# Optimization experiments

Hardware: AMD Instinct MI355X
Metric: run time of the kernel (lower is better)

Reference implementation:

```python
import jax, jax.numpy as jnp
import numpy as np

B_SZ, CH, H, W = 32, 256, 28, 28
D_INNER, D_STATE, D_CONV, DT_RANK, DEPTH = 512, 16, 4, 16, 2


def setup_inputs() -> dict:
    key = jax.random.key(0)
    ks = jax.random.split(key, 10)
    s = 0.02
    A = jnp.broadcast_to(jnp.arange(1, D_STATE + 1, dtype=jnp.float32), (DEPTH, D_INNER, D_STATE))
    return {
        "bbox_feats": jax.random.normal(ks[0], (B_SZ, CH, H, W), jnp.float32),
        "norm_w": jnp.ones((DEPTH, CH), jnp.float32),
        "norm_b": jnp.zeros((DEPTH, CH), jnp.float32),
        "in_proj_w": jax.random.normal(ks[1], (DEPTH, 2 * D_INNER, CH), jnp.float32) * s,
        "conv_w": jax.random.normal(ks[2], (DEPTH, D_INNER, D_CONV), jnp.float32) * 0.1,
        "conv_b": jnp.zeros((DEPTH, D_INNER), jnp.float32),
        "x_proj_w": jax.random.normal(ks[3], (DEPTH, DT_RANK + 2 * D_STATE, D_INNER), jnp.float32) * s,
        "dt_proj_w": jax.random.normal(ks[4], (DEPTH, D_INNER, DT_RANK), jnp.float32) * 0.1,
        "dt_proj_b": jax.random.normal(ks[5], (DEPTH, D_INNER), jnp.float32) * 0.1,
        "A_log": jnp.log(A),
        "D_param": jnp.ones((DEPTH, D_INNER), jnp.float32),
        "out_proj_w": jax.random.normal(ks[6], (DEPTH, CH, D_INNER), jnp.float32) * s,
    }


def _layernorm(x, w, b, eps=1e-5):
    mu = jnp.mean(x, axis=-1, keepdims=True)
    var = jnp.mean(jnp.square(x - mu), axis=-1, keepdims=True)
    return (x - mu) * jax.lax.rsqrt(var + eps) * w + b


def _mamba(x, in_w, cw, cb, xp_w, dtp_w, dtp_b, A_log, Dp, out_w):
    # x: [B, L, d_model]
    B, L, _ = x.shape
    xz = jnp.einsum('bld,ed->ble', x, in_w)          # [B, L, 2*d_inner]
    xi, z = jnp.split(xz, 2, axis=-1)                # each [B, L, d_inner]
    # depthwise causal conv1d (kernel D_CONV, left pad D_CONV-1)
    xpad = jnp.pad(xi, ((0, 0), (D_CONV - 1, 0), (0, 0)))
    xc = cb
    for k in range(D_CONV):
        xc = xc + xpad[:, k:k + L, :] * cw[:, k]
    xc = jax.nn.silu(xc)                             # [B, L, d_inner]
    x_dbl = jnp.einsum('bld,ed->ble', xc, xp_w)      # [B, L, dt_rank+2*d_state]
    dt_r = x_dbl[..., :DT_RANK]
    Bm = x_dbl[..., DT_RANK:DT_RANK + D_STATE]
    Cm = x_dbl[..., DT_RANK + D_STATE:]
    dt = jax.nn.softplus(jnp.einsum('blr,dr->bld', dt_r, dtp_w) + dtp_b)  # [B, L, d_inner]
    A = -jnp.exp(A_log)                              # [d_inner, d_state]

    def step(h, inp):
        dt_t, B_t, C_t, x_t = inp                    # [B,d_inner],[B,d_state],[B,d_state],[B,d_inner]
        dA = jnp.exp(dt_t[:, :, None] * A)           # [B, d_inner, d_state]
        h = h * dA + dt_t[:, :, None] * B_t[:, None, :] * x_t[:, :, None]
        y = jnp.einsum('bds,bs->bd', h, C_t)
        return h, y

    h0 = jnp.zeros((B, D_INNER, D_STATE), x.dtype)
    inputs = (jnp.swapaxes(dt, 0, 1), jnp.swapaxes(Bm, 0, 1),
              jnp.swapaxes(Cm, 0, 1), jnp.swapaxes(xc, 0, 1))
    _, ys = jax.lax.scan(step, h0, inputs)
    y = jnp.swapaxes(ys, 0, 1) + xc * Dp             # [B, L, d_inner]
    y = y * jax.nn.silu(z)
    return jnp.einsum('bld,ed->ble', y, out_w)       # [B, L, d_model]


def reference(bbox_feats, norm_w, norm_b, in_proj_w, conv_w, conv_b,
              x_proj_w, dt_proj_w, dt_proj_b, A_log, D_param, out_proj_w):
    B, C, h, w = bbox_feats.shape
    x = bbox_feats
    for i in range(DEPTH):
        xf = jnp.swapaxes(x.reshape(B, C, h * w), -1, -2)   # [B, L, C]
        xn = _layernorm(xf, norm_w[i], norm_b[i])
        ym = _mamba(xn, in_proj_w[i], conv_w[i], conv_b[i], x_proj_w[i],
                    dt_proj_w[i], dt_proj_b[i], A_log[i], D_param[i], out_proj_w[i])
        x = jnp.swapaxes(ym, -1, -2).reshape(B, C, h, w)
    return x
```

## Files before the change

kernel.cpp:

```cpp
#include <hip/hip_runtime.h>
#include <cstdint>
#include <cstddef>

#define BSZ  32
#define CHN  256
#define LSEQ 784
#define DI   512
#define NCH  16

typedef unsigned short u16;
typedef short s16x8 __attribute__((ext_vector_type(8)));
typedef float f32x4 __attribute__((ext_vector_type(4)));

__device__ __forceinline__ float b2f(u16 u) {
  union { unsigned int i; float f; } v; v.i = ((unsigned int)u) << 16; return v.f;
}
__device__ __forceinline__ u16 f2b(float f) {
  union { float f; unsigned int i; } v; v.f = f;
  unsigned int x = v.i;
  return (u16)((x + 0x7FFFu + ((x >> 16) & 1u)) >> 16);
}

#define SA_HALF(dv, xv, Q0, Q1, Q2, Q3) do {                                  \
  float dx_ = (dv) * (xv);                                                    \
  float w1_ = __expf(-(dv));                                                  \
  float e2_ = w1_*w1_, e4_ = e2_*e2_, e8_ = e4_*e4_;                          \
  float p3_ = e2_*w1_, p5_ = e4_*w1_, p6_ = e4_*e2_, p7_ = p6_*w1_;           \
  float p9_ = e8_*w1_, p10_ = e8_*e2_, p11_ = p10_*w1_, p12_ = e8_*e4_;       \
  float p13_ = p12_*w1_, p14_ = p12_*e2_, p15_ = p14_*w1_, p16_ = e8_*e8_;    \
  h[0]  = h[0]*w1_  + dx_*Q0.x;  h[1]  = h[1]*e2_  + dx_*Q0.y;                \
  h[2]  = h[2]*p3_  + dx_*Q0.z;  h[3]  = h[3]*e4_  + dx_*Q0.w;                \
  h[4]  = h[4]*p5_  + dx_*Q1.x;  h[5]  = h[5]*p6_  + dx_*Q1.y;                \
  h[6]  = h[6]*p7_  + dx_*Q1.z;  h[7]  = h[7]*e8_  + dx_*Q1.w;                \
  h[8]  = h[8]*p9_  + dx_*Q2.x;  h[9]  = h[9]*p10_ + dx_*Q2.y;                \
  h[10] = h[10]*p11_+ dx_*Q2.z;  h[11] = h[11]*p12_+ dx_*Q2.w;                \
  h[12] = h[12]*p13_+ dx_*Q3.x;  h[13] = h[13]*p14_+ dx_*Q3.y;                \
  h[14] = h[14]*p15_+ dx_*Q3.z;  h[15] = h[15]*p16_+ dx_*Q3.w;                \
} while (0)

#define SC_HALF(dv, xv, zv, Q0, Q1, Q2, Q3, R0, R1, R2, R3, YB) do {          \
  SA_HALF(dv, xv, Q0, Q1, Q2, Q3);                                            \
  float ya_ = h[0]*R0.x;  ya_ = fmaf(h[1], R0.y, ya_);                        \
  ya_ = fmaf(h[2], R0.z, ya_);  ya_ = fmaf(h[3], R0.w, ya_);                  \
  float yb_ = h[4]*R1.x;  yb_ = fmaf(h[5], R1.y, yb_);                        \
  yb_ = fmaf(h[6], R1.z, yb_);  yb_ = fmaf(h[7], R1.w, yb_);                  \
  float yc_ = h[8]*R2.x;  yc_ = fmaf(h[9], R2.y, yc_);                        \
  yc_ = fmaf(h[10], R2.z, yc_); yc_ = fmaf(h[11], R2.w, yc_);                 \
  float yd_ = h[12]*R3.x; yd_ = fmaf(h[13], R3.y, yd_);                       \
  yd_ = fmaf(h[14], R3.z, yd_); yd_ = fmaf(h[15], R3.w, yd_);                 \
  float yy_ = (ya_ + yb_) + (yc_ + yd_) + (xv) * dpar;                        \
  float sg_ = (zv) / (1.f + __expf(-(zv)));                                   \
  YB = f2b(yy_ * sg_);                                                        \
} while (0)

__global__ void k_flag(const unsigned* __restrict__ nwraw, int* __restrict__ flag) {
  if (threadIdx.x == 0 && blockIdx.x == 0) {
    flag[0] = (nwraw[0] == 0x3F803F80u) ? 1 : 0;
    flag[1] = 1;
  }
}

__global__ __launch_bounds__(256) void k_canon(const void* __restrict__ src,
                                               u16* __restrict__ dst, int n,
                                               const int* __restrict__ flag) {
  int i = blockIdx.x * 2048 + threadIdx.x;
  if (flag[0]) {
    const u16* s = (const u16*)src;
#pragma unroll
    for (int q = 0; q < 8; q++) {
      int j = i + q * 256;
      if (j < n) dst[j] = s[j];
    }
  } else {
    const float* s = (const float*)src;
#pragma unroll
    for (int q = 0; q < 8; q++) {
      int j = i + q * 256;
      if (j < n) dst[j] = f2b(s[j]);
    }
  }
}

__global__ __launch_bounds__(256) void k_norm(const void* __restrict__ xv,
                                              int b0,
                                              const int* __restrict__ flag,
                                              const u16* __restrict__ nw,
                                              const u16* __restrict__ nb,
                                              u16* __restrict__ xn) {
  bool isbf = flag[0] != 0;
  int b  = blockIdx.y;
  int gb = b0 + b;
  int l0 = blockIdx.x * 64;
  int tx = threadIdx.x & 63;
  int ty = threadIdx.x >> 6;
  int l  = l0 + tx;
  bool valid = l < LSEQ;
  const u16*   xb16 = (const u16*)xv   + (size_t)gb * CHN * LSEQ;
  const float* xb32 = (const float*)xv + (size_t)gb * CHN * LSEQ;
  float s = 0.f, sq = 0.f;
  for (int c = ty; c < CHN; c += 4) {
    size_t idx = (size_t)c * LSEQ + l;
    float v = 0.f;
    if (valid) v = isbf ? b2f(xb16[idx]) : xb32[idx];
    s += v; sq += v * v;
  }
  __shared__ float rs[4][64], rq[4][64], smu[64], srs[64];
  rs[ty][tx] = s; rq[ty][tx] = sq;
  __syncthreads();
  if (ty == 0) {
    float ss = rs[0][tx] + rs[1][tx] + rs[2][tx] + rs[3][tx];
    float qq = rq[0][tx] + rq[1][tx] + rq[2][tx] + rq[3][tx];
    float mu  = ss * (1.f / CHN);
    float var = qq * (1.f / CHN) - mu * mu;
    smu[tx] = mu;
    srs[tx] = rsqrtf(var + 1e-5f);
  }
  __syncthreads();
  if (valid) {
    float mu = smu[tx], rstd = srs[tx];
    u16* xnb = xn + (size_t)b * CHN * LSEQ;
    for (int c = ty; c < CHN; c += 4) {
      size_t idx = (size_t)c * LSEQ + l;
      float v = isbf ? b2f(xb16[idx]) : xb32[idx];
      xnb[idx] = f2b((v - mu) * rstd * b2f(nw[c]) + b2f(nb[c]));
    }
  }
}

template <int MODE>
__global__ __launch_bounds__(256) void k_gmm(const u16* __restrict__ A,
                                             const u16* __restrict__ W,
                                             float* __restrict__ C0,
                                             u16* __restrict__ Cb0,
                                             u16* __restrict__ Cb1,
                                             void* __restrict__ Dout,
                                             const int* __restrict__ flag,
                                             int b0, int K, int Ntot) {
  __shared__ unsigned ldsA[128 * 20];
  __shared__ unsigned ldsW[64 * 20];
  int tid = threadIdx.x;
  int m0 = blockIdx.x * 128;
  int n0 = blockIdx.y * 64;
  int b  = blockIdx.z;
  int w    = tid >> 6;
  int l15  = tid & 15;
  int quad = (tid >> 4) & 3;
  int kp = tid & 15;
  int mo = tid >> 4;
  int wn = tid >> 2;
  int wc = tid & 3;

  const u16* Ab = A + (size_t)b * K * LSEQ;

  f32x4 acc[8];
#pragma unroll
  for (int i = 0; i < 8; i++)
#pragma unroll
    for (int r = 0; r < 4; r++) acc[i][r] = 0.f;

  for (int k0 = 0; k0 < K; k0 += 32) {
    __syncthreads();
    {
      int mg = m0 + mo * 8;
      unsigned lo[4] = {0u, 0u, 0u, 0u}, hi[4] = {0u, 0u, 0u, 0u};
      if (mg < LSEQ) {
        int4 r0 = *(const int4*)(Ab + (size_t)(k0 + 2 * kp) * LSEQ + mg);
        int4 r1 = *(const int4*)(Ab + (size_t)(k0 + 2 * kp + 1) * LSEQ + mg);
        lo[0] = (unsigned)r0.x; lo[1] = (unsigned)r0.y;
        lo[2] = (unsigned)r0.z; lo[3] = (unsigned)r0.w;
        hi[0] = (unsigned)r1.x; hi[1] = (unsigned)r1.y;
        hi[2] = (unsigned)r1.z; hi[3] = (unsigned)r1.w;
      }
#pragma unroll
      for (int j = 0; j < 8; j++) {
        unsigned lov = (lo[j >> 1] >> ((j & 1) * 16)) & 0xFFFFu;
        unsigned hiv = (hi[j >> 1] >> ((j & 1) * 16)) & 0xFFFFu;
        ldsA[(mo * 8 + j) * 20 + kp] = lov | (hiv << 16);
      }
    }
    {
      int ng = n0 + wn;
      int4 r = make_int4(0, 0, 0, 0);
      if (ng < Ntot) r = *(const int4*)(W + (size_t)ng * K + k0 + wc * 8);
      *(int4*)(ldsW + wn * 20 + wc * 4) = r;
    }
    __syncthreads();
    s16x8 bf = *(const s16x8*)(ldsW + ((w * 16 + l15) * 20 + quad * 4));
#pragma unroll
    for (int mi = 0; mi < 8; mi++) {
      s16x8 af = *(const s16x8*)(ldsA + ((mi * 16 + l15) * 20 + quad * 4));
      acc[mi] = __builtin_amdgcn_mfma_f32_16x16x32_bf16(af, bf, acc[mi], 0, 0, 0);
    }
  }

  int n_g = n0 + w * 16 + l15;
  if (n_g >= Ntot) return;
#pragma unroll
  for (int mi = 0; mi < 8; mi++) {
    int mb = m0 + mi * 16;
    if (mb >= LSEQ) break;
    int m = mb + quad * 4;
    float v0 = acc[mi][0], v1 = acc[mi][1], v2 = acc[mi][2], v3 = acc[mi][3];
    if constexpr (MODE == 0) {
      if (n_g < 16) {
        float* crow = C0 + ((size_t)b * Ntot + n_g) * LSEQ + m;
        *(float4*)crow = make_float4(v0, v1, v2, v3);
      } else {
        float* bcf = (float*)Dout;
        size_t rbase = ((size_t)b * LSEQ + m) * 32 + (n_g - 16);
        bcf[rbase]      = v0;
        bcf[rbase + 32] = v1;
        bcf[rbase + 64] = v2;
        bcf[rbase + 96] = v3;
      }
    } else if constexpr (MODE == 3) {
      size_t off = ((size_t)(b0 + b) * Ntot + n_g) * LSEQ + m;
      if (flag[0]) {
        u16* crow = (u16*)Dout + off;
        ((unsigned*)crow)[0] = (unsigned)f2b(v0) | ((unsigned)f2b(v1) << 16);
        ((unsigned*)crow)[1] = (unsigned)f2b(v2) | ((unsigned)f2b(v3) << 16);
      } else {
        float* crow = (float*)Dout + off;
        *(float4*)crow = make_float4(v0, v1, v2, v3);
      }
    } else {
      u16* crow;
      if constexpr (MODE == 1) {
        crow = (n_g < DI) ? (Cb0 + ((size_t)b * DI + n_g) * LSEQ + m)
                          : (Cb1 + ((size_t)b * DI + (n_g - DI)) * LSEQ + m);
      } else {
        crow = Cb0 + ((size_t)b * Ntot + n_g) * LSEQ + m;
      }
      ((unsigned*)crow)[0] = (unsigned)f2b(v0) | ((unsigned)f2b(v1) << 16);
      ((unsigned*)crow)[1] = (unsigned)f2b(v2) | ((unsigned)f2b(v3) << 16);
    }
  }
}

__global__ __launch_bounds__(256) void k_conv(const u16* __restrict__ xi,
                                              const u16* __restrict__ cw,
                                              const u16* __restrict__ cb,
                                              u16* __restrict__ xc) {
  int b = blockIdx.z, e = blockIdx.y;
  int l = blockIdx.x * 256 + threadIdx.x;
  if (l >= LSEQ) return;
  const u16* xr = xi + ((size_t)b * DI + e) * LSEQ;
  float acc = b2f(cb[e]);
#pragma unroll
  for (int k = 0; k < 4; k++) {
    int li = l - 3 + k;
    if (li >= 0) acc += b2f(xr[li]) * b2f(cw[e * 4 + k]);
  }
  acc = acc / (1.f + __expf(-acc));
  xc[((size_t)b * DI + e) * LSEQ + l] = f2b(acc);
}

__device__ __forceinline__ float softplus_f(float x) {
  float t = __expf(x);
  return (x > 20.f) ? x : __logf(1.f + t);
}

__global__ __launch_bounds__(256) void k_dtp(const float* __restrict__ xd,
                                             const u16* __restrict__ dtw,
                                             const u16* __restrict__ dtbv,
                                             u16* __restrict__ dtp) {
  __shared__ float Ls[16][64];
  int b  = blockIdx.y;
  int l0 = blockIdx.x * 64;
  int tid = threadIdx.x;
  const float* xb = xd + (size_t)b * 48 * LSEQ;
  for (int idx = tid; idx < 16 * 64; idx += 256) {
    int r = idx >> 6, lo = idx & 63;
    int l = l0 + lo;
    Ls[r][lo] = (l < LSEQ) ? xb[(size_t)r * LSEQ + l] : 0.f;
  }
  __syncthreads();
  int tx = tid & 63, ty = tid >> 6;
  int l = l0 + tx;
  if (l >= LSEQ) return;
  u16* drow = dtp + (size_t)b * DI * LSEQ + l;
  for (int eg = 0; eg < 128; eg++) {
    int e = ty * 128 + eg;
    float acc = b2f(dtbv[e]);
#pragma unroll
    for (int r = 0; r < 16; r++) acc += Ls[r][tx] * b2f(dtw[e * 16 + r]);
    drow[(size_t)e * LSEQ] = f2b(softplus_f(acc));
  }
}

__global__ __launch_bounds__(256, 2) void k_scanA(const u16* __restrict__ dtp,
                                                  const float* __restrict__ BC,
                                                  const u16* __restrict__ xc,
                                                  const u16* __restrict__ A_log,
                                                  float* __restrict__ Sb,
                                                  float* __restrict__ hloc) {
  __shared__ unsigned xs[256 * 13];
  __shared__ unsigned ds[256 * 13];
  __shared__ float bcsA[26 * 4 * 16];
  int tid = threadIdx.x;
  int b = blockIdx.x >> 5;
  int r = blockIdx.x & 31;
  int e     = ((r >> 2) << 6) + (tid & 63);
  int cq    = r & 3;
  int w     = tid >> 6;
  int chunk = cq * 4 + w;
  bool pow_ok = true;
#pragma unroll
  for (int n = 0; n < 16; n++) {
    float an = -__expf(b2f(A_log[e * 16 + n]));
    pow_ok = pow_ok && (fabsf(an + (float)(n + 1)) < 0.02f * (n + 1));
  }
  float h[16];
#pragma unroll
  for (int n = 0; n < 16; n++) h[n] = 0.f;
  float S = 0.f;
  int lbase = chunk * 50;
  const unsigned* gx = (const unsigned*)(xc  + ((size_t)b * DI + e) * LSEQ + lbase);
  const unsigned* gd = (const unsigned*)(dtp + ((size_t)b * DI + e) * LSEQ + lbase);
  unsigned* myx = xs + tid * 13;
  unsigned* myd = ds + tid * 13;
  float a[16];
  if (!pow_ok) {
#pragma unroll
    for (int n = 0; n < 16; n++) a[n] = -__expf(b2f(A_log[e * 16 + n]));
  }
#pragma unroll
  for (int t = 0; t < 2; t++) {
    int nd = (t == 0) ? 13 : ((chunk == 15) ? 4 : 12);
    const unsigned* gxo = gx + t * 13;
    const unsigned* gdo = gd + t * 13;
    for (int j = 0; j < nd; j++) { myx[j] = gxo[j]; myd[j] = gdo[j]; }
    int NS = (t == 0) ? 26 : 24;
    int total = NS * 64;
    for (int k = 0; k < 7; k++) {
      int lin = tid + k * 256;
      if (lin < total) {
        int q = lin & 15;
        int rest = lin >> 4;
        int wc = rest & 3;
        int s = rest >> 2;
        int l = (cq * 4 + wc) * 50 + t * 26 + s;
        bcsA[lin] = BC[((size_t)b * LSEQ + l) * 32 + q];
      }
    }
    __syncthreads();
    if (pow_ok) {
      for (int j = 0; j < nd; j++) {
        unsigned wd = myd[j], wx = myx[j];
        float d0 = b2f((u16)(wd & 0xFFFFu)), x0 = b2f((u16)(wx & 0xFFFFu));
        float d1 = b2f((u16)(wd >> 16)),     x1 = b2f((u16)(wx >> 16));
        const float4* bp0 = (const float4*)(bcsA + (((2 * j) * 4 + w) << 4));
        float4 P0 = bp0[0], P1 = bp0[1], P2 = bp0[2], P3 = bp0[3];
        const float4* bp1 = (const float4*)(bcsA + (((2 * j + 1) * 4 + w) << 4));
        float4 Q0 = bp1[0], Q1 = bp1[1], Q2 = bp1[2], Q3 = bp1[3];
        S += d0;
        SA_HALF(d0, x0, P0, P1, P2, P3);
        S += d1;
        SA_HALF(d1, x1, Q0, Q1, Q2, Q3);
      }
    } else {
      for (int j = 0; j < nd; j++) {
        unsigned wd = myd[j], wx = myx[j];
        for (int hs = 0; hs < 2; hs++) {
          float d  = b2f((u16)(hs ? (wd >> 16) : (wd & 0xFFFFu)));
          float xt = b2f((u16)(hs ? (wx >> 16) : (wx & 0xFFFFu)));
          S += d;
          const float4* bp = (const float4*)(bcsA + (((2 * j + hs) * 4 + w) << 4));
          float4 B0 = bp[0], B1 = bp[1], B2 = bp[2], B3 = bp[3];
          float Bv[16] = {B0.x,B0.y,B0.z,B0.w, B1.x,B1.y,B1.z,B1.w,
                          B2.x,B2.y,B2.z,B2.w, B3.x,B3.y,B3.z,B3.w};
          float dx = d * xt;
#pragma unroll
          for (int n = 0; n < 16; n++) {
            float da = __expf(d * a[n]);
            h[n] = h[n] * da + dx * Bv[n];
          }
        }
      }
    }
    __syncthreads();
  }
  Sb[((size_t)b * DI + e) * NCH + chunk] = S;
  size_t base = (((size_t)b * DI + e) * NCH + chunk) * 16;
  float4* Hp = (float4*)(hloc + base);
#pragma unroll
  for (int q = 0; q < 4; q++)
    Hp[q] = make_float4(h[q*4], h[q*4+1], h[q*4+2], h[q*4+3]);
}

__global__ __launch_bounds__(256) void k_comb(const u16* __restrict__ A_log,
                                              const float* __restrict__ Sb,
                                              float* hloc) {
  int idx = blockIdx.x * 256 + threadIdx.x;
  int n  = idx & 15;
  int be = idx >> 4;
  int e  = be & (DI - 1);
  float an = -__expf(b2f(A_log[e * 16 + n]));
  size_t hbase = (size_t)be * (NCH * 16) + n;
  size_t sbase = (size_t)be * NCH;
  float h = 0.f;
#pragma unroll
  for (int c = 0; c < NCH; c++) {
    size_t o = hbase + (size_t)c * 16;
    float hl = hloc[o];
    float p  = __expf(an * Sb[sbase + c]);
    hloc[o] = h;
    h = hl + p * h;
  }
}

__global__ __launch_bounds__(256, 2) void k_scanC(const u16* __restrict__ dtp,
                                                  const float* __restrict__ BC,
                                                  const u16* __restrict__ zp,
                                                  const u16* __restrict__ A_log,
                                                  const u16* __restrict__ Dp,
                                                  const float* __restrict__ hinit,
                                                  u16* xcy) {
  __shared__ unsigned xs[256 * 13];
  __shared__ unsigned zs[256 * 13];
  __shared__ unsigned ds[256 * 13];
  __shared__ float bcsC[26 * 4 * 32];
  int tid = threadIdx.x;
  int b = blockIdx.x >> 5;
  int r = blockIdx.x & 31;
  int e     = ((r >> 2) << 6) + (tid & 63);
  int cq    = r & 3;
  int w     = tid >> 6;
  int chunk = cq * 4 + w;
  bool pow_ok = true;
#pragma unroll
  for (int n = 0; n < 16; n++) {
    float an = -__expf(b2f(A_log[e * 16 + n]));
    pow_ok = pow_ok && (fabsf(an + (float)(n + 1)) < 0.02f * (n + 1));
  }
  float h[16];
  {
    size_t base = (((size_t)b * DI + e) * NCH + chunk) * 16;
    const float4* Hp = (const float4*)(hinit + base);
#pragma unroll
    for (int q = 0; q < 4; q++) {
      float4 v = Hp[q];
      h[q*4] = v.x; h[q*4+1] = v.y; h[q*4+2] = v.z; h[q*4+3] = v.w;
    }
  }
  float dpar = b2f(Dp[e]);
  int lbase = chunk * 50;
  unsigned* gy        = (unsigned*)(xcy + ((size_t)b * DI + e) * LSEQ + lbase);
  const unsigned* gz  = (const unsigned*)(zp  + ((size_t)b * DI + e) * LSEQ + lbase);
  const unsigned* gd  = (const unsigned*)(dtp + ((size_t)b * DI + e) * LSEQ + lbase);
  unsigned* myx = xs + tid * 13;
  unsigned* myz = zs + tid * 13;
  unsigned* myd = ds + tid * 13;
  float a[16];
  if (!pow_ok) {
#pragma unroll
    for (int n = 0; n < 16; n++) a[n] = -__expf(b2f(A_log[e * 16 + n]));
  }
#pragma unroll
  for (int t = 0; t < 2; t++) {
    int nd = (t == 0) ? 13 : ((chunk == 15) ? 4 : 12);
    const unsigned* gxo = gy + t * 13;
    const unsigned* gzo = gz + t * 13;
    const unsigned* gdo = gd + t * 13;
    for (int j = 0; j < nd; j++) {
      myx[j] = gxo[j]; myz[j] = gzo[j]; myd[j] = gdo[j];
    }
    int NS = (t == 0) ? 26 : 24;
    int total = NS * 128;
    for (int k = 0; k < 13; k++) {
      int lin = tid + k * 256;
      if (lin < total) {
        int q = lin & 31;
        int rest = lin >> 5;
        int wc = rest & 3;
        int s = rest >> 2;
        int l = (cq * 4 + wc) * 50 + t * 26 + s;
        bcsC[lin] = BC[((size_t)b * LSEQ + l) * 32 + q];
      }
    }
    __syncthreads();
    unsigned* gyo = gy + t * 13;
    if (pow_ok) {
      for (int j = 0; j < nd; j++) {
        unsigned wd = myd[j], wx = myx[j], wz = myz[j];
        float d0 = b2f((u16)(wd & 0xFFFFu)), x0 = b2f((u16)(wx & 0xFFFFu)),
              z0 = b2f((u16)(wz & 0xFFFFu));
        float d1 = b2f((u16)(wd >> 16)),     x1 = b2f((u16)(wx >> 16)),
              z1 = b2f((u16)(wz >> 16));
        const float4* bp0 = (const float4*)(bcsC + (((2 * j) * 4 + w) << 5));
        float4 P0 = bp0[0], P1 = bp0[1], P2 = bp0[2], P3 = bp0[3];
        float4 R0 = bp0[4], R1 = bp0[5], R2 = bp0[6], R3 = bp0[7];
        const float4* bp1 = (const float4*)(bcsC + (((2 * j + 1) * 4 + w) << 5));
        float4 Q0 = bp1[0], Q1 = bp1[1], Q2 = bp1[2], Q3 = bp1[3];
        float4 T0 = bp1[4], T1 = bp1[5], T2 = bp1[6], T3 = bp1[7];
        u16 y0, y1;
        SC_HALF(d0, x0, z0, P0, P1, P2, P3, R0, R1, R2, R3, y0);
        SC_HALF(d1, x1, z1, Q0, Q1, Q2, Q3, T0, T1, T2, T3, y1);
        myx[j] = (unsigned)y0 | ((unsigned)y1 << 16);
      }
    } else {
      for (int j = 0; j < nd; j++) {
        unsigned wd = myd[j], wx = myx[j], wz = myz[j];
        unsigned ypk = 0u;
        for (int hs = 0; hs < 2; hs++) {
          float d  = b2f((u16)(hs ? (wd >> 16) : (wd & 0xFFFFu)));
          float xt = b2f((u16)(hs ? (wx >> 16) : (wx & 0xFFFFu)));
          float z  = b2f((u16)(hs ? (wz >> 16) : (wz & 0xFFFFu)));
          const float4* bp = (const float4*)(bcsC + (((2 * j + hs) * 4 + w) << 5));
          float4 B0 = bp[0], B1 = bp[1], B2 = bp[2], B3 = bp[3];
          float4 C0 = bp[4], C1 = bp[5], C2 = bp[6], C3 = bp[7];
          float Bv[16] = {B0.x,B0.y,B0.z,B0.w, B1.x,B1.y,B1.z,B1.w,
                          B2.x,B2.y,B2.z,B2.w, B3.x,B3.y,B3.z,B3.w};
          float Cv[16] = {C0.x,C0.y,C0.z,C0.w, C1.x,C1.y,C1.z,C1.w,
                          C2.x,C2.y,C2.z,C2.w, C3.x,C3.y,C3.z,C3.w};
          float dx = d * xt;
          float yacc = 0.f;
#pragma unroll
          for (int n = 0; n < 16; n++) {
            float da = __expf(d * a[n]);
            h[n] = h[n] * da + dx * Bv[n];
            yacc += h[n] * Cv[n];
          }
          float yy = yacc + xt * dpar;
          float sg = 1.f / (1.f + __expf(-z));
          u16 yb = f2b(yy * (z * sg));
          ypk |= ((unsigned)yb) << (16 * hs);
        }
        myx[j] = ypk;
      }
    }
    for (int j = 0; j < nd; j++) gyo[j] = myx[j];
    __syncthreads();
  }
}

extern "C" void kernel_launch(void* const* d_in, const int* in_sizes, int n_in,
                              void* d_out, int out_size, void* d_ws, size_t ws_size,
                              hipStream_t stream) {
  u16* ws = (u16*)d_ws;

  u16* c_nw  = ws;
  u16* c_nb  = ws + 512;
  u16* c_inw = ws + 1024;
  u16* c_cw  = ws + 525312;
  u16* c_cb  = ws + 529408;
  u16* c_xpw = ws + 530432;
  u16* c_dtw = ws + 579584;
  u16* c_dtb = ws + 595968;
  u16* c_al  = ws + 596992;
  u16* c_dp  = ws + 613376;
  u16* c_ow  = ws + 614400;
  int* flag  = (int*)(ws + 876544);
  const size_t WREG = 876552;

  k_flag<<<1, 64, 0, stream>>>((const unsigned*)d_in[1], flag);
  {
    const void* srcs[11] = {d_in[1], d_in[2], d_in[3], d_in[4], d_in[5], d_in[6],
                            d_in[7], d_in[8], d_in[9], d_in[10], d_in[11]};
    u16* dsts[11] = {c_nw, c_nb, c_inw, c_cw, c_cb, c_xpw,
                     c_dtw, c_dtb, c_al, c_dp, c_ow};
    int ns[11] = {512, 512, 524288, 4096, 1024, 49152,
                  16384, 1024, 16384, 1024, 262144};
    for (int k = 0; k < 11; k++)
      k_canon<<<(ns[k] + 2047) / 2048, 256, 0, stream>>>(srcs[k], dsts[k], ns[k], flag);
  }

  size_t fixed_bytes = WREG * 2;
  size_t per_batch   = 4ull * DI * LSEQ * 2;
  int Bg = 1;
  for (int g = 32; g >= 1; g >>= 1) {
    if (ws_size >= fixed_bytes + (size_t)g * per_batch) { Bg = g; break; }
  }

  size_t plane = (size_t)Bg * DI * LSEQ;
  u16*   pb = ws + WREG;
  u16*   xi = pb;
  float* fb = (float*)pb;
  float* bc = fb;
  float* xd = bc + (size_t)Bg * LSEQ * 32;
  float* Sb = xd;
  float* hl = Sb + (size_t)Bg * DI * NCH;
  u16*   zp = pb + plane;
  u16*   xc = pb + 2 * plane;
  u16*   dtx1 = pb + 3 * plane;
  u16*   dtp = dtx1;
  u16*   x1  = dtx1;
  u16*   xn = xc;

  for (int b0 = 0; b0 < BSZ; b0 += Bg) {
    for (int i = 0; i < 2; i++) {
      if (i == 0)
        k_norm<<<dim3(13, Bg), 256, 0, stream>>>(
            d_in[0], b0, flag, c_nw, c_nb, xn);
      else
        k_norm<<<dim3(13, Bg), 256, 0, stream>>>(
            (const void*)x1, 0, flag + 1, c_nw + CHN, c_nb + CHN, xn);
      k_gmm<1><<<dim3(7, 16, Bg), 256, 0, stream>>>(
          xn, c_inw + (size_t)i * 1024 * CHN, nullptr, xi, zp,
          nullptr, nullptr, 0, CHN, 1024);
      k_conv<<<dim3(4, 512, Bg), 256, 0, stream>>>(
          xi, c_cw + i * DI * 4, c_cb + i * DI, xc);
      k_gmm<0><<<dim3(7, 1, Bg), 256, 0, stream>>>(
          xc, c_xpw + (size_t)i * 48 * DI, xd, nullptr, nullptr,
          (void*)bc, nullptr, 0, DI, 48);
      k_dtp<<<dim3(13, Bg), 256, 0, stream>>>(
          xd, c_dtw + i * DI * 16, c_dtb + i * DI, dtp);
      k_scanA<<<Bg * 32, 256, 0, stream>>>(
          dtp, bc, xc, c_al + i * DI * 16, Sb, hl);
      k_comb<<<Bg * 32, 256, 0, stream>>>(c_al + i * DI * 16, Sb, hl);
      k_scanC<<<Bg * 32, 256, 0, stream>>>(
          dtp, bc, zp, c_al + i * DI * 16, c_dp + i * DI, hl, xc);
      if (i == 0)
        k_gmm<2><<<dim3(7, 4, Bg), 256, 0, stream>>>(
            xc, c_ow, nullptr, x1, nullptr,
            nullptr, nullptr, 0, DI, CHN);
      else
        k_gmm<3><<<dim3(7, 4, Bg), 256, 0, stream>>>(
            xc, c_ow + (size_t)CHN * DI, nullptr, nullptr, nullptr,
            d_out, flag, b0, DI, CHN);
    }
  }
}
```

Before: 879.3 us.

## Write normalized activations in GEMM-tiled packed layout and merge canon launches

The layernorm kernel now writes its output as channel pairs packed into 32-bit words, grouped in 128-position tiles. This lets the in-projection GEMM (MODE 1) load its A operand with contiguous 16-byte reads and no bounds check or repacking. The eleven per-parameter conversion launches are also merged into one kernel that finds its segment from a block-prefix table. Risks: the last tile past L=784 reads padding that may be uninitialized, and the norm kernel's stores now have a different coalescing pattern.

```diff
diff --git a/kernel.cpp b/kernel.cpp
--- a/kernel.cpp
+++ b/kernel.cpp
@@ -7,6 +7,10 @@
 #define LSEQ 784
 #define DI   512
 #define NCH  16
+
+#define PK_TILE  16384
+#define PK_NT    7
+#define PK_PERB  (PK_NT * PK_TILE)
 
 typedef unsigned short u16;
 typedef short s16x8 __attribute__((ext_vector_type(8)));
@@ -60,23 +64,37 @@
   }
 }
 
-__global__ __launch_bounds__(256) void k_canon(const void* __restrict__ src,
-                                               u16* __restrict__ dst, int n,
-                                               const int* __restrict__ flag) {
-  int i = blockIdx.x * 2048 + threadIdx.x;
+struct CanonSrcs { const void* p[11]; };
+
+__global__ __launch_bounds__(256) void k_canon_all(CanonSrcs s,
+                                                   u16* __restrict__ ws,
+                                                   const int* __restrict__ flag) {
+  const int ns[11]  = {512, 512, 524288, 4096, 1024, 49152,
+                       16384, 1024, 16384, 1024, 262144};
+  const int off[11] = {0, 512, 1024, 525312, 529408, 530432,
+                       579584, 595968, 596992, 613376, 614400};
+  const int pre[12] = {0, 1, 2, 258, 260, 261, 285, 293, 294, 302, 303, 431};
+  int bid = blockIdx.x;
+  int seg = 0;
+#pragma unroll
+  for (int k = 1; k < 11; k++) if (bid >= pre[k]) seg = k;
+  int lb = bid - pre[seg];
+  int n = ns[seg];
+  u16* dst = ws + off[seg];
+  int i = lb * 2048 + threadIdx.x;
   if (flag[0]) {
-    const u16* s = (const u16*)src;
+    const u16* src = (const u16*)s.p[seg];
 #pragma unroll
     for (int q = 0; q < 8; q++) {
       int j = i + q * 256;
-      if (j < n) dst[j] = s[j];
+      if (j < n) dst[j] = src[j];
     }
   } else {
-    const float* s = (const float*)src;
+    const float* src = (const float*)s.p[seg];
 #pragma unroll
     for (int q = 0; q < 8; q++) {
       int j = i + q * 256;
-      if (j < n) dst[j] = f2b(s[j]);
+      if (j < n) dst[j] = f2b(src[j]);
     }
   }
 }
@@ -118,11 +136,17 @@
   __syncthreads();
   if (valid) {
     float mu = smu[tx], rstd = srs[tx];
-    u16* xnb = xn + (size_t)b * CHN * LSEQ;
-    for (int c = ty; c < CHN; c += 4) {
-      size_t idx = (size_t)c * LSEQ + l;
-      float v = isbf ? b2f(xb16[idx]) : xb32[idx];
-      xnb[idx] = f2b((v - mu) * rstd * b2f(nw[c]) + b2f(nb[c]));
+    unsigned* Pp = (unsigned*)xn + (size_t)b * PK_PERB
+                 + (size_t)(l >> 7) * PK_TILE + (l & 127);
+    for (int kp = ty; kp < 128; kp += 4) {
+      int c0 = 2 * kp, c1 = c0 + 1;
+      size_t i0 = (size_t)c0 * LSEQ + l;
+      size_t i1 = (size_t)c1 * LSEQ + l;
+      float v0 = isbf ? b2f(xb16[i0]) : xb32[i0];
+      float v1 = isbf ? b2f(xb16[i1]) : xb32[i1];
+      u16 a0 = f2b((v0 - mu) * rstd * b2f(nw[c0]) + b2f(nb[c0]));
+      u16 a1 = f2b((v1 - mu) * rstd * b2f(nw[c1]) + b2f(nb[c1]));
+      Pp[(size_t)kp * 128] = (unsigned)a0 | ((unsigned)a1 << 16);
     }
   }
 }
@@ -150,8 +174,6 @@
   int wn = tid >> 2;
   int wc = tid & 3;
 
-  const u16* Ab = A + (size_t)b * K * LSEQ;
-
   f32x4 acc[8];
 #pragma unroll
   for (int i = 0; i < 8; i++)
@@ -160,7 +182,21 @@
 
   for (int k0 = 0; k0 < K; k0 += 32) {
     __syncthreads();
-    {
+    if constexpr (MODE == 1) {
+      int mo2 = tid & 15;
+      int kpp = tid >> 4;
+      const unsigned* Pb = (const unsigned*)A + (size_t)b * PK_PERB
+                         + (size_t)blockIdx.x * PK_TILE
+                         + (size_t)((k0 >> 1) + kpp) * 128 + mo2 * 8;
+      int4 r0 = *(const int4*)Pb;
+      int4 r1 = *(const int4*)(Pb + 4);
+      unsigned vals[8] = {(unsigned)r0.x, (unsigned)r0.y, (unsigned)r0.z, (unsigned)r0.w,
+                          (unsigned)r1.x, (unsigned)r1.y, (unsigned)r1.z, (unsigned)r1.w};
+#pragma unroll
+      for (int q = 0; q < 8; q++)
+        ldsA[(mo2 * 8 + q) * 20 + kpp] = vals[q];
+    } else {
+      const u16* Ab = A + (size_t)b * K * LSEQ;
       int mg = m0 + mo * 8;
       unsigned lo[4] = {0u, 0u, 0u, 0u}, hi[4] = {0u, 0u, 0u, 0u};
       if (mg < LSEQ) {
@@ -555,14 +591,9 @@
 
   k_flag<<<1, 64, 0, stream>>>((const unsigned*)d_in[1], flag);
   {
-    const void* srcs[11] = {d_in[1], d_in[2], d_in[3], d_in[4], d_in[5], d_in[6],
-                            d_in[7], d_in[8], d_in[9], d_in[10], d_in[11]};
-    u16* dsts[11] = {c_nw, c_nb, c_inw, c_cw, c_cb, c_xpw,
-                     c_dtw, c_dtb, c_al, c_dp, c_ow};
-    int ns[11] = {512, 512, 524288, 4096, 1024, 49152,
-                  16384, 1024, 16384, 1024, 262144};
-    for (int k = 0; k < 11; k++)
-      k_canon<<<(ns[k] + 2047) / 2048, 256, 0, stream>>>(srcs[k], dsts[k], ns[k], flag);
+    CanonSrcs s;
+    for (int k = 0; k < 11; k++) s.p[k] = d_in[k + 1];
+    k_canon_all<<<431, 256, 0, stream>>>(s, ws, flag);
   }
 
   size_t fixed_bytes = WREG * 2;
```

After: 894.2 us. No clear change (+1.7%).
